# Optimization experiments

Measured on AMD Instinct MI355X. Metric: run time of the kernel, lower is better.

Reference implementation:

```python
import jax, jax.numpy as jnp
from jax import lax
import numpy as np

NUM_P0 = 512  # Decoder.num_p0


def conv1(w, b, x):
    # 1x1 Conv1d: w (O,I), x (B,I,N) -> (B,O,N)
    return jnp.einsum('oi,bin->bon', w, x) + b[None, :, None]


def mlp_res(w1, b1, w2, b2, ws, bs, x):
    # MLP_Res: conv2(relu(conv1(x))) + shortcut(x)
    return conv1(w2, b2, jax.nn.relu(conv1(w1, b1, x))) + conv1(ws, bs, x)


def fps_subsample(points, n_samples):
    # Farthest point sampling, matching pointnet2 CUDA semantics (start at idx 0).
    # points: (B, N, 3) -> (B, n_samples, 3)
    B, N, _ = points.shape
    init_d = jnp.full((B, N), 1e10, dtype=points.dtype)
    init_idx = jnp.zeros((B,), dtype=jnp.int32)

    def step(carry, _):
        d, last_idx = carry
        last_pt = jnp.take_along_axis(points, last_idx[:, None, None], axis=1)  # (B,1,3)
        dist = jnp.sum((points - last_pt) ** 2, axis=-1)  # (B,N)
        d = jnp.minimum(d, dist)
        nxt = jnp.argmax(d, axis=-1).astype(jnp.int32)
        return (d, nxt), last_idx

    _, idxs = lax.scan(step, (init_d, init_idx), None, length=n_samples)
    idxs = idxs.T  # (B, n_samples)
    return jnp.take_along_axis(points, idxs[..., None], axis=1)


def setup_inputs() -> dict:
    key = jax.random.key(0)
    ks = jax.random.split(key, 32)
    s = 0.05
    inp = {
        'feat':    jax.random.normal(ks[0], (32, 512, 1), jnp.float32),
        'partial': jax.random.normal(ks[1], (32, 32768, 3), jnp.float32),
        'ps_w':  jax.random.normal(ks[2], (512, 128, 256), jnp.float32) * s,
        'ps_b':  jax.random.normal(ks[3], (128,), jnp.float32) * s,
        'm1_w1': jax.random.normal(ks[4], (128, 640), jnp.float32) * s,
        'm1_b1': jax.random.normal(ks[5], (128,), jnp.float32) * s,
        'm1_w2': jax.random.normal(ks[6], (128, 128), jnp.float32) * s,
        'm1_b2': jax.random.normal(ks[7], (128,), jnp.float32) * s,
        'm1_ws': jax.random.normal(ks[8], (128, 640), jnp.float32) * s,
        'm1_bs': jax.random.normal(ks[9], (128,), jnp.float32) * s,
        'm2_w1': jax.random.normal(ks[10], (64, 128), jnp.float32) * s,
        'm2_b1': jax.random.normal(ks[11], (64,), jnp.float32) * s,
        'm2_w2': jax.random.normal(ks[12], (128, 64), jnp.float32) * s,
        'm2_b2': jax.random.normal(ks[13], (128,), jnp.float32) * s,
        'm2_ws': jax.random.normal(ks[14], (128, 128), jnp.float32) * s,
        'm2_bs': jax.random.normal(ks[15], (128,), jnp.float32) * s,
        'm3_w1': jax.random.normal(ks[16], (128, 640), jnp.float32) * s,
        'm3_b1': jax.random.normal(ks[17], (128,), jnp.float32) * s,
        'm3_w2': jax.random.normal(ks[18], (128, 128), jnp.float32) * s,
        'm3_b2': jax.random.normal(ks[19], (128,), jnp.float32) * s,
        'm3_ws': jax.random.normal(ks[20], (128, 640), jnp.float32) * s,
        'm3_bs': jax.random.normal(ks[21], (128,), jnp.float32) * s,
        'm4_w1': jax.random.normal(ks[22], (64, 128), jnp.float32) * s,
        'm4_b1': jax.random.normal(ks[23], (64,), jnp.float32) * s,
        'm4_w2': jax.random.normal(ks[24], (3, 64), jnp.float32) * s,
        'm4_b2': jax.random.normal(ks[25], (3,), jnp.float32) * s,
    }
    return inp


def reference(feat, partial, ps_w, ps_b,
              m1_w1, m1_b1, m1_w2, m1_b2, m1_ws, m1_bs,
              m2_w1, m2_b1, m2_w2, m2_b2, m2_ws, m2_bs,
              m3_w1, m3_b1, m3_w2, m3_b2, m3_ws, m3_bs,
              m4_w1, m4_b1, m4_w2, m4_b2):
    f = feat[:, :, 0]                                   # (B, 512)
    # ConvTranspose1d(512,128,256) on length-1 input == einsum over kernel dim
    x1 = jnp.einsum('bi,iok->bok', f, ps_w) + ps_b[None, :, None]  # (B,128,256)
    n = x1.shape[2]
    fr = jnp.broadcast_to(feat, (feat.shape[0], feat.shape[1], n))  # (B,512,256)
    x1 = mlp_res(m1_w1, m1_b1, m1_w2, m1_b2, m1_ws, m1_bs, jnp.concatenate([x1, fr], axis=1))
    x2 = mlp_res(m2_w1, m2_b1, m2_w2, m2_b2, m2_ws, m2_bs, x1)
    x3 = mlp_res(m3_w1, m3_b1, m3_w2, m3_b2, m3_ws, m3_bs, jnp.concatenate([x2, fr], axis=1))
    completion = conv1(m4_w2, m4_b2, jax.nn.relu(conv1(m4_w1, m4_b1, x3)))  # (B,3,256)
    pcd = jnp.transpose(completion, (0, 2, 1))          # (B,256,3) coarse seeds
    p0 = fps_subsample(jnp.concatenate([pcd, partial], axis=1), NUM_P0)  # (B,512,3)
    return pcd, p0
```

## Files before the change

kernel.cpp:

```cpp
#include <hip/hip_runtime.h>

#define NFULL 33024
#define FPS_T 512
#define BST   99072

__global__ void k_ps(const float* __restrict__ feat,
                     const float* __restrict__ psw,
                     const float* __restrict__ psb,
                     float* __restrict__ out)
{
    __shared__ float fs[16384];
    const int tid = threadIdx.x;
    for (int k = tid; k < 16384; k += 256) fs[k] = feat[k];
    __syncthreads();
    const int col = blockIdx.x * 256 + tid;
    float acc[32];
    #pragma unroll
    for (int b = 0; b < 32; ++b) acc[b] = 0.f;
    for (int i = 0; i < 512; i += 4) {
        const float w0 = psw[(i+0)*32768 + col];
        const float w1 = psw[(i+1)*32768 + col];
        const float w2 = psw[(i+2)*32768 + col];
        const float w3 = psw[(i+3)*32768 + col];
        #pragma unroll
        for (int b = 0; b < 32; ++b) {
            const float4 f4 = *(const float4*)&fs[b*512 + i];
            acc[b] += f4.x*w0 + f4.y*w1 + f4.z*w2 + f4.w*w3;
        }
    }
    const float bias = psb[col >> 8];
    #pragma unroll
    for (int b = 0; b < 32; ++b) out[b*32768 + col] = acc[b] + bias;
}

__global__ void k_fb(const float* __restrict__ feat,
                     const float* __restrict__ wa, const float* __restrict__ wb,
                     const float* __restrict__ wc, const float* __restrict__ wd,
                     float* __restrict__ fb)
{
    const int tid = blockIdx.x * 256 + threadIdx.x;
    const int wsel = tid >> 12;
    const int r = tid & 4095;
    const int b = r >> 7, o = r & 127;
    const float* w = (wsel == 0 ? wa : wsel == 1 ? wb : wsel == 2 ? wc : wd) + o*640 + 128;
    const float* f = feat + b*512;
    float acc = 0.f;
    for (int i = 0; i < 512; i += 4) {
        const float4 wv = *(const float4*)(w + i);
        const float4 fv = *(const float4*)(f + i);
        acc += wv.x*fv.x + wv.y*fv.y + wv.z*fv.z + wv.w*fv.w;
    }
    fb[tid] = acc;
}

__global__ void k_conv(const float* __restrict__ x,
                       const float* __restrict__ w,
                       const float* __restrict__ bias,
                       const float* __restrict__ fb,
                       const float* __restrict__ add,
                       float* __restrict__ out,
                       const int O, const int K, const int ldw, const int relu)
{
    const int bo = blockIdx.x;
    const int b = bo / O;
    const int o = bo - b * O;
    const int n = threadIdx.x;
    const float* __restrict__ wr = w + o * ldw;
    const float* __restrict__ xb = x + (b * K) * 256 + n;
    float acc = 0.f;
    for (int i = 0; i < K; i += 4) {
        const float4 wv = *(const float4*)(wr + i);
        acc += wv.x * xb[(i+0) << 8];
        acc += wv.y * xb[(i+1) << 8];
        acc += wv.z * xb[(i+2) << 8];
        acc += wv.w * xb[(i+3) << 8];
    }
    acc += bias[o];
    if (fb)   acc += fb[b * O + o];
    if (add)  acc += add[bo * 256 + n];
    if (relu) acc = fmaxf(acc, 0.f);
    out[bo * 256 + n] = acc;
}

__global__ void k_pcd(const float* __restrict__ comp,
                      float* __restrict__ pcd_out,
                      float* __restrict__ XYZ)
{
    const int tid = blockIdx.x * 256 + threadIdx.x;
    const int b = tid >> 8, n = tid & 255;
    const float cx = comp[(b*3+0)*256 + n];
    const float cy = comp[(b*3+1)*256 + n];
    const float cz = comp[(b*3+2)*256 + n];
    pcd_out[tid*3+0] = cx; pcd_out[tid*3+1] = cy; pcd_out[tid*3+2] = cz;
    float* Xb = XYZ + b*BST;
    Xb[n]           = cx;
    Xb[33024  + n]  = cy;
    Xb[66048  + n]  = cz;
}

__global__ void k_copy(const float* __restrict__ partial, float* __restrict__ XYZ)
{
    const int p = blockIdx.x*256 + threadIdx.x;
    const int b = p >> 15, i = p & 32767;
    const float x = partial[p*3+0];
    const float y = partial[p*3+1];
    const float z = partial[p*3+2];
    float* Xb = XYZ + b*BST;
    Xb[256 + i]          = x;
    Xb[33024 + 256 + i]  = y;
    Xb[66048 + 256 + i]  = z;
}


#define REP16(M) \
  M(0) M(1) M(2) M(3) M(4) M(5) M(6) M(7) \
  M(8) M(9) M(10) M(11) M(12) M(13) M(14) M(15)

#define FBODY(xx, yy, zz, dd, cc) { \
    const float dx = __fsub_rn((xx), lx); \
    const float dy = __fsub_rn((yy), ly); \
    const float dz = __fsub_rn((zz), lz); \
    const float dist = __fadd_rn(__fadd_rn(__fmul_rn(dx,dx), __fmul_rn(dy,dy)), \
                                 __fmul_rn(dz,dz)); \
    dd = fminf(dd, dist); \
    if (dd > bestv) { bestv = dd; bestc = (cc); } }

#define FPS_GRP(jo) { \
    const int off = (jo)*2048 + t4; \
    const float4 x4 = *(const float4*)(Xb + off); \
    const float4 y4 = *(const float4*)(Yb + off); \
    const float4 z4 = *(const float4*)(Zb + off); \
    float4 d4 = *(float4*)(dls + off); \
    FBODY(x4.x, y4.x, z4.x, d4.x, (jo)*4 + 0) \
    FBODY(x4.y, y4.y, z4.y, d4.y, (jo)*4 + 1) \
    FBODY(x4.z, y4.z, z4.z, d4.z, (jo)*4 + 2) \
    FBODY(x4.w, y4.w, z4.w, d4.w, (jo)*4 + 3) \
    *(float4*)(dls + off) = d4; }

__launch_bounds__(FPS_T)
__global__ void k_fps(const float* __restrict__ XYZ, float* __restrict__ outp)
{
    __shared__ __align__(16) float dls[NFULL];
    __shared__ float redv[2][8];
    __shared__ int   redi[2][8];

    const int b = blockIdx.x;
    const int t = threadIdx.x;
    const int t4 = t << 2;
    const float* __restrict__ Xb = XYZ + b*BST;
    const float* __restrict__ Yb = Xb + 33024;
    const float* __restrict__ Zb = Xb + 66048;
    const float NEG = -__builtin_inff();

    {
        const float4 v = make_float4(1.0e10f, 1.0e10f, 1.0e10f, 1.0e10f);
        #pragma unroll
        for (int jo = 0; jo < 16; ++jo) *(float4*)(dls + jo*2048 + t4) = v;
        if (t < 64) *(float4*)(dls + 32768 + t4) = v;
    }
    __syncthreads();

    int last = 0;
    float* __restrict__ po = outp + b * (512*3);
    for (int s = 0; s < 512; ++s) {
        const float lx = Xb[last];
        const float ly = Yb[last];
        const float lz = Zb[last];
        if (t == 0) { po[s*3+0] = lx; po[s*3+1] = ly; po[s*3+2] = lz; }
        if (s == 511) break;

        float bestv = NEG;
        int   bestc = 0x7FFFFFFF;
        REP16(FPS_GRP)
        if (t < 64) {
            const int off = 32768 + t4;
            const float4 x4 = *(const float4*)(Xb + off);
            const float4 y4 = *(const float4*)(Yb + off);
            const float4 z4 = *(const float4*)(Zb + off);
            float4 d4 = *(float4*)(dls + off);
            FBODY(x4.x, y4.x, z4.x, d4.x, 64)
            FBODY(x4.y, y4.y, z4.y, d4.y, 65)
            FBODY(x4.z, y4.z, z4.z, d4.z, 66)
            FBODY(x4.w, y4.w, z4.w, d4.w, 67)
            *(float4*)(dls + off) = d4;
        }
        int besti = ((bestc >> 2) << 11) + t4 + (bestc & 3);

        #pragma unroll
        for (int m = 1; m < 64; m <<= 1) {
            const float ov = __shfl_xor(bestv, m, 64);
            const int   oi = __shfl_xor(besti, m, 64);
            if (ov > bestv || (ov == bestv && oi < besti)) { bestv = ov; besti = oi; }
        }
        const int bank = s & 1;
        if ((t & 63) == 0) { redv[bank][t >> 6] = bestv; redi[bank][t >> 6] = besti; }
        __syncthreads();
        {
            const int lane = t & 63;
            float v = (lane < 8) ? redv[bank][lane] : NEG;
            int   i = (lane < 8) ? redi[bank][lane] : 0x7FFFFFFF;
            #pragma unroll
            for (int m = 1; m < 8; m <<= 1) {
                const float ov = __shfl_xor(v, m, 64);
                const int   oi = __shfl_xor(i, m, 64);
                if (ov > v || (ov == v && oi < i)) { v = ov; i = oi; }
            }
            last = __shfl(i, 0, 64);
        }
    }
}

extern "C" void kernel_launch(void* const* d_in, const int* in_sizes, int n_in,
                              void* d_out, int out_size, void* d_ws, size_t ws_size,
                              hipStream_t stream)
{
    const float* feat    = (const float*)d_in[0];
    const float* partial = (const float*)d_in[1];
    const float* ps_w    = (const float*)d_in[2];
    const float* ps_b    = (const float*)d_in[3];
    const float* m1_w1   = (const float*)d_in[4];
    const float* m1_b1   = (const float*)d_in[5];
    const float* m1_w2   = (const float*)d_in[6];
    const float* m1_b2   = (const float*)d_in[7];
    const float* m1_ws   = (const float*)d_in[8];
    const float* m1_bs   = (const float*)d_in[9];
    const float* m2_w1   = (const float*)d_in[10];
    const float* m2_b1   = (const float*)d_in[11];
    const float* m2_w2   = (const float*)d_in[12];
    const float* m2_b2   = (const float*)d_in[13];
    const float* m2_ws   = (const float*)d_in[14];
    const float* m2_bs   = (const float*)d_in[15];
    const float* m3_w1   = (const float*)d_in[16];
    const float* m3_b1   = (const float*)d_in[17];
    const float* m3_w2   = (const float*)d_in[18];
    const float* m3_b2   = (const float*)d_in[19];
    const float* m3_ws   = (const float*)d_in[20];
    const float* m3_bs   = (const float*)d_in[21];
    const float* m4_w1   = (const float*)d_in[22];
    const float* m4_b1   = (const float*)d_in[23];
    const float* m4_w2   = (const float*)d_in[24];
    const float* m4_b2   = (const float*)d_in[25];

    float* ws = (float*)d_ws;
    float* XYZ = ws;
    float* A  = ws + 3170304;
    float* B  = ws + 4218880;
    float* C  = ws + 5267456;
    float* FB = ws + 6316032;

    float* out = (float*)d_out;

    k_ps  <<<128,  256, 0, stream>>>(feat, ps_w, ps_b, A);
    k_fb  <<<64,   256, 0, stream>>>(feat, m1_w1, m1_ws, m3_w1, m3_ws, FB);
    k_copy<<<4096, 256, 0, stream>>>(partial, XYZ);

    k_conv<<<32*128, 256, 0, stream>>>(A, m1_w1, m1_b1, FB,       nullptr, B, 128, 128, 640, 1);
    k_conv<<<32*128, 256, 0, stream>>>(A, m1_ws, m1_bs, FB+4096,  nullptr, C, 128, 128, 640, 0);
    k_conv<<<32*128, 256, 0, stream>>>(B, m1_w2, m1_b2, nullptr,  C,       A, 128, 128, 128, 0);
    k_conv<<<32*64,  256, 0, stream>>>(A, m2_w1, m2_b1, nullptr,  nullptr, B, 64,  128, 128, 1);
    k_conv<<<32*128, 256, 0, stream>>>(A, m2_ws, m2_bs, nullptr,  nullptr, C, 128, 128, 128, 0);
    k_conv<<<32*128, 256, 0, stream>>>(B, m2_w2, m2_b2, nullptr,  C,       A, 128, 64,  64,  0);
    k_conv<<<32*128, 256, 0, stream>>>(A, m3_w1, m3_b1, FB+8192,  nullptr, B, 128, 128, 640, 1);
    k_conv<<<32*128, 256, 0, stream>>>(A, m3_ws, m3_bs, FB+12288, nullptr, C, 128, 128, 640, 0);
    k_conv<<<32*128, 256, 0, stream>>>(B, m3_w2, m3_b2, nullptr,  C,       A, 128, 128, 128, 0);
    k_conv<<<32*64,  256, 0, stream>>>(A, m4_w1, m4_b1, nullptr,  nullptr, B, 64,  128, 128, 1);
    k_conv<<<32*3,   256, 0, stream>>>(B, m4_w2, m4_b2, nullptr,  nullptr, C, 3,   64,  64,  0);

    k_pcd <<<32, 256, 0, stream>>>(C, out, XYZ);
    k_fps <<<32, FPS_T, 0, stream>>>(XYZ, out + 24576);
}
```

Measured before the change: 2.139 ms.

## Stage part of FPS z-coordinates in LDS and use packed float2 arithmetic

The FPS inner loop now computes squared distances with two-wide float vectors (packed FP32 ops), with FMA contraction disabled so rounding still matches the reference. The first 6144 z-coordinates of each batch are copied once into shared memory and read from there in every iteration, which cuts repeated global/L2 traffic for that slice. The trade-off is extra LDS use, which may lower occupancy, and a one-time copy cost.

```diff
diff --git a/kernel.cpp b/kernel.cpp
--- a/kernel.cpp
+++ b/kernel.cpp
@@ -3,6 +3,9 @@
 #define NFULL 33024
 #define FPS_T 512
 #define BST   99072
+
+typedef float v2f __attribute__((ext_vector_type(2)));
+static __device__ __forceinline__ v2f mk2(float a, float b) { v2f r; r.x = a; r.y = b; return r; }
 
 __global__ void k_ps(const float* __restrict__ feat,
                      const float* __restrict__ psw,
@@ -112,10 +115,6 @@
 }
 
 
-#define REP16(M) \
-  M(0) M(1) M(2) M(3) M(4) M(5) M(6) M(7) \
-  M(8) M(9) M(10) M(11) M(12) M(13) M(14) M(15)
-
 #define FBODY(xx, yy, zz, dd, cc) { \
     const float dx = __fsub_rn((xx), lx); \
     const float dy = __fsub_rn((yy), ly); \
@@ -125,22 +124,35 @@
     dd = fminf(dd, dist); \
     if (dd > bestv) { bestv = dd; bestc = (cc); } }
 
-#define FPS_GRP(jo) { \
+#define FPS_GRP(jo, ZP) { \
     const int off = (jo)*2048 + t4; \
     const float4 x4 = *(const float4*)(Xb + off); \
     const float4 y4 = *(const float4*)(Yb + off); \
-    const float4 z4 = *(const float4*)(Zb + off); \
+    const float4 z4 = *(const float4*)((ZP) + off); \
     float4 d4 = *(float4*)(dls + off); \
-    FBODY(x4.x, y4.x, z4.x, d4.x, (jo)*4 + 0) \
-    FBODY(x4.y, y4.y, z4.y, d4.y, (jo)*4 + 1) \
-    FBODY(x4.z, y4.z, z4.z, d4.z, (jo)*4 + 2) \
-    FBODY(x4.w, y4.w, z4.w, d4.w, (jo)*4 + 3) \
-    *(float4*)(dls + off) = d4; }
+    v2f da, db; \
+    { \
+      _Pragma("clang fp contract(off)") \
+      const v2f dxa = mk2(x4.x, x4.y) - lx2, dxb = mk2(x4.z, x4.w) - lx2; \
+      const v2f dya = mk2(y4.x, y4.y) - ly2, dyb = mk2(y4.z, y4.w) - ly2; \
+      const v2f dza = mk2(z4.x, z4.y) - lz2, dzb = mk2(z4.z, z4.w) - lz2; \
+      const v2f sa = (dxa*dxa + dya*dya) + dza*dza; \
+      const v2f sb = (dxb*dxb + dyb*dyb) + dzb*dzb; \
+      da = __builtin_elementwise_min(mk2(d4.x, d4.y), sa); \
+      db = __builtin_elementwise_min(mk2(d4.z, d4.w), sb); \
+    } \
+    d4.x = da.x; d4.y = da.y; d4.z = db.x; d4.w = db.y; \
+    *(float4*)(dls + off) = d4; \
+    if (da.x > bestv) { bestv = da.x; bestc = (jo)*4 + 0; } \
+    if (da.y > bestv) { bestv = da.y; bestc = (jo)*4 + 1; } \
+    if (db.x > bestv) { bestv = db.x; bestc = (jo)*4 + 2; } \
+    if (db.y > bestv) { bestv = db.y; bestc = (jo)*4 + 3; } }
 
 __launch_bounds__(FPS_T)
 __global__ void k_fps(const float* __restrict__ XYZ, float* __restrict__ outp)
 {
     __shared__ __align__(16) float dls[NFULL];
+    __shared__ __align__(16) float zls[6144];
     __shared__ float redv[2][8];
     __shared__ int   redi[2][8];
 
@@ -157,6 +169,7 @@
         #pragma unroll
         for (int jo = 0; jo < 16; ++jo) *(float4*)(dls + jo*2048 + t4) = v;
         if (t < 64) *(float4*)(dls + 32768 + t4) = v;
+        for (int k = t; k < 6144; k += FPS_T) zls[k] = Zb[k];
     }
     __syncthreads();
 
@@ -168,10 +181,15 @@
         const float lz = Zb[last];
         if (t == 0) { po[s*3+0] = lx; po[s*3+1] = ly; po[s*3+2] = lz; }
         if (s == 511) break;
+        const v2f lx2 = mk2(lx, lx), ly2 = mk2(ly, ly), lz2 = mk2(lz, lz);
 
         float bestv = NEG;
         int   bestc = 0x7FFFFFFF;
-        REP16(FPS_GRP)
+        FPS_GRP(0, zls) FPS_GRP(1, zls) FPS_GRP(2, zls)
+        FPS_GRP(3, Zb)  FPS_GRP(4, Zb)  FPS_GRP(5, Zb)  FPS_GRP(6, Zb)
+        FPS_GRP(7, Zb)  FPS_GRP(8, Zb)  FPS_GRP(9, Zb)  FPS_GRP(10, Zb)
+        FPS_GRP(11, Zb) FPS_GRP(12, Zb) FPS_GRP(13, Zb) FPS_GRP(14, Zb)
+        FPS_GRP(15, Zb)
         if (t < 64) {
             const int off = 32768 + t4;
             const float4 x4 = *(const float4*)(Xb + off);
```

New measurement: 2.144 ms. Within noise of the previous version (+0.3%).
